# Optimization experiments

Measured on AMD Instinct MI355X. Metric: run time of the kernel, lower is better.

The kernel has to match this reference:

```python
import jax, jax.numpy as jnp
import numpy as np

B, H0, W0, DIM, HEADS, WS, SHIFT = 32, 56, 56, 384, 12, 7, 3
MLP_HID = DIM * 4
N = WS * WS  # tokens per window

def _rel_pos_index(ws):
    coords = np.stack(np.meshgrid(np.arange(ws), np.arange(ws), indexing='ij')).reshape(2, -1)
    rel = (coords[:, :, None] - coords[:, None, :]).transpose(1, 2, 0)
    rel[:, :, 0] += ws - 1
    rel[:, :, 1] += ws - 1
    rel[:, :, 0] *= 2 * ws - 1
    return rel.sum(-1)  # (N, N) int

REL_IDX = _rel_pos_index(WS)

def _shift_mask(H, W, ws, shift):
    # standard Swin SW-MSA mask: 0 within same region, -100 across regions
    img = np.zeros((H, W), dtype=np.int32)
    cnt = 0
    for hs in (slice(0, -ws), slice(-ws, -shift), slice(-shift, None)):
        for wsl in (slice(0, -ws), slice(-ws, -shift), slice(-shift, None)):
            img[hs, wsl] = cnt
            cnt += 1
    mw = img.reshape(H // ws, ws, W // ws, ws).transpose(0, 2, 1, 3).reshape(-1, ws * ws)
    return np.where(mw[:, None, :] != mw[:, :, None], -100.0, 0.0).astype(np.float32)  # (nW, N, N)

MASK = _shift_mask(H0, W0, WS, SHIFT)

def _ln(x, g, b, eps=1e-5):
    m = x.mean(-1, keepdims=True)
    v = ((x - m) ** 2).mean(-1, keepdims=True)
    return (x - m) / jnp.sqrt(v + eps) * g + b

def setup_inputs():
    key = jax.random.key(0)
    ks = jax.random.split(key, 8)
    d = {}
    d['x'] = jax.random.normal(ks[0], (B, H0 * W0, DIM), jnp.float32)
    d['H'], d['W'] = H0, W0
    d['norm1_g'] = jnp.ones((DIM,), jnp.float32)
    d['norm1_b'] = jnp.zeros((DIM,), jnp.float32)
    d['qkv_w'] = jax.random.normal(ks[1], (3 * DIM, DIM), jnp.float32) * 0.02
    d['qkv_b'] = jnp.zeros((3 * DIM,), jnp.float32)
    d['rpb_table'] = jax.random.normal(ks[2], ((2 * WS - 1) ** 2, HEADS), jnp.float32) * 0.02
    d['proj_w'] = jax.random.normal(ks[3], (DIM, DIM), jnp.float32) * 0.02
    d['proj_b'] = jnp.zeros((DIM,), jnp.float32)
    d['norm2_g'] = jnp.ones((DIM,), jnp.float32)
    d['norm2_b'] = jnp.zeros((DIM,), jnp.float32)
    d['fc1_w'] = jax.random.normal(ks[4], (MLP_HID, DIM), jnp.float32) * 0.02
    d['fc1_b'] = jnp.zeros((MLP_HID,), jnp.float32)
    d['fc2_w'] = jax.random.normal(ks[5], (DIM, MLP_HID), jnp.float32) * 0.02
    d['fc2_b'] = jnp.zeros((DIM,), jnp.float32)
    return d

def reference(x, H, W, norm1_g, norm1_b, qkv_w, qkv_b, rpb_table, proj_w, proj_b, norm2_g, norm2_b, fc1_w, fc1_b, fc2_w, fc2_b):
    Bx, L, C = x.shape
    hd = C // HEADS
    scale = hd ** -0.5
    shortcut = x
    xn = _ln(x, norm1_g, norm1_b).reshape(Bx, H, W, C)
    if SHIFT > 0:
        xn = jnp.roll(xn, (-SHIFT, -SHIFT), axis=(1, 2))
    nWh, nWw = H // WS, W // WS
    nW = nWh * nWw
    # window partition: (B, H, W, C) -> (B*nW, N, C)
    xw = xn.reshape(Bx, nWh, WS, nWw, WS, C).transpose(0, 1, 3, 2, 4, 5).reshape(-1, N, C)
    qkv = (xw @ qkv_w.T + qkv_b).reshape(-1, N, 3, HEADS, hd).transpose(2, 0, 3, 1, 4)
    q, k, v = qkv[0] * scale, qkv[1], qkv[2]  # (B*nW, HEADS, N, hd)
    attn = jnp.einsum('bhnd,bhmd->bhnm', q, k)
    bias = rpb_table[jnp.asarray(REL_IDX.reshape(-1))].reshape(N, N, HEADS).transpose(2, 0, 1)
    attn = attn + bias[None]
    if SHIFT > 0:
        attn = attn.reshape(Bx, nW, HEADS, N, N) + jnp.asarray(MASK)[None, :, None]
        attn = attn.reshape(-1, HEADS, N, N)
    attn = jax.nn.softmax(attn, axis=-1)
    out = jnp.einsum('bhnm,bhmd->bhnd', attn, v).transpose(0, 2, 1, 3).reshape(-1, N, C)
    out = out @ proj_w.T + proj_b
    # window reverse: (B*nW, N, C) -> (B, H, W, C)
    xr = out.reshape(Bx, nWh, nWw, WS, WS, C).transpose(0, 1, 3, 2, 4, 5).reshape(Bx, H, W, C)
    if SHIFT > 0:
        xr = jnp.roll(xr, (SHIFT, SHIFT), axis=(1, 2))
    x = shortcut + xr.reshape(Bx, L, C)
    h = _ln(x, norm2_g, norm2_b)
    h = jax.nn.gelu(h @ fc1_w.T + fc1_b, approximate=False)  # nn.GELU default = exact erf
    h = h @ fc2_w.T + fc2_b
    return x + h
```

## Files before the change

### kernel.cpp

```cpp
#include <hip/hip_runtime.h>
#include <hip/hip_bf16.h>

#define C_DIM   384
#define HEADS   12
#define HDIM    32
#define NTOK    49
#define TOT_WIN 2048
#define M_TOK   100352
#define QKV_N   1152
#define MLP_N   1536
#define SHIFT_V 3

typedef __bf16 bf16x8_t __attribute__((ext_vector_type(8)));
typedef float  f32x4_t  __attribute__((ext_vector_type(4)));

__device__ inline float b2f(ushort u) {
    union { unsigned u; float f; } p; p.u = ((unsigned)u) << 16; return p.f;
}
__device__ inline ushort f2b(float f) {
    union { float f; unsigned u; } p; p.f = f;
    unsigned r = p.u + 0x7FFF + ((p.u >> 16) & 1);
    return (ushort)(r >> 16);
}
__device__ inline float ldin(const void* p, size_t i, int dt) {
    return dt ? b2f(((const ushort*)p)[i]) : ((const float*)p)[i];
}

__device__ inline void gload_lds16(const ushort* g, ushort* l) {
    __builtin_amdgcn_global_load_lds(
        (__attribute__((address_space(1))) void*)const_cast<ushort*>(g),
        (__attribute__((address_space(3))) void*)l, 16, 0, 0);
}

__device__ inline int win2tok(int grow) {
    int widx = grow / 49, tok = grow - widx * 49;
    int b = widx >> 6, w_ = widx & 63;
    int wh = w_ >> 3, ww = w_ & 7;
    int r = tok / 7, c = tok - r * 7;
    int h = wh * 7 + r + SHIFT_V; if (h >= 56) h -= 56;
    int wc = ww * 7 + c + SHIFT_V; if (wc >= 56) wc -= 56;
    return b * 3136 + h * 56 + wc;
}

__global__ void sniff_kernel(const ushort* x16, int* flag) {
    const int tid = threadIdx.x;
    int cnt = 0;
    for (int i = tid; i < 4096; i += 256) {
        ushort u = x16[2 * i];
        int e = (u >> 7) & 0xFF;
        if ((u & 0x7FFF) == 0 || (e >= 107 && e <= 147)) cnt++;
    }
    __shared__ int ss[256];
    ss[tid] = cnt; __syncthreads();
    for (int s = 128; s; s >>= 1) { if (tid < s) ss[tid] += ss[tid + s]; __syncthreads(); }
    if (tid == 0) *flag = (ss[0] >= 2048) ? 1 : 0;
}

__global__ void cvt_w_kernel(const void* src, ushort* dst, int n, const int* flagp) {
    const int dt = *flagp;
    for (int i = blockIdx.x * blockDim.x + threadIdx.x; i < n; i += gridDim.x * blockDim.x)
        dst[i] = dt ? ((const ushort*)src)[i] : f2b(((const float*)src)[i]);
}

__global__ void cvt_p_kernel(const void* n1g, const void* n1b, const void* qkvb,
                             const void* projb, const void* n2g, const void* n2b,
                             const void* fc1b, const void* fc2b, const void* rpb,
                             float* prm, const int* flagp) {
    const int dt = *flagp;
    for (int i = threadIdx.x; i < 7020; i += 256) {
        float v;
        if      (i < 384)  v = ldin(n1g,  i,        dt);
        else if (i < 768)  v = ldin(n1b,  i - 384,  dt);
        else if (i < 1920) v = ldin(qkvb, i - 768,  dt);
        else if (i < 2304) v = ldin(projb,i - 1920, dt);
        else if (i < 2688) v = ldin(n2g,  i - 2304, dt);
        else if (i < 3072) v = ldin(n2b,  i - 2688, dt);
        else if (i < 4608) v = ldin(fc1b, i - 3072, dt);
        else if (i < 4992) v = ldin(fc2b, i - 4608, dt);
        else               v = ldin(rpb,  i - 4992, dt);
        prm[i] = v;
    }
}

template<int MODE>
__global__ __launch_bounds__(256) void ln_kernel(
    const void* __restrict__ x, const float* __restrict__ g,
    const float* __restrict__ b, ushort* __restrict__ out,
    const int* flagp, int moff)
{
    const int dt = *flagp;
    const int wid = threadIdx.x >> 6, lane = threadIdx.x & 63;
    const int m = blockIdx.x * 4 + wid;
    const int src = (MODE == 0) ? win2tok(moff + m) : (moff + m);

    float v[6]; float s = 0.f, sq = 0.f;
    #pragma unroll
    for (int k = 0; k < 6; ++k) {
        size_t idx = (size_t)src * C_DIM + lane + 64 * k;
        v[k] = (MODE == 2) ? b2f(((const ushort*)x)[idx]) : ldin(x, idx, dt);
        s += v[k]; sq += v[k] * v[k];
    }
    #pragma unroll
    for (int off = 32; off; off >>= 1) {
        s  += __shfl_xor(s,  off, 64);
        sq += __shfl_xor(sq, off, 64);
    }
    float mean = s * (1.f / 384.f);
    float var  = sq * (1.f / 384.f) - mean * mean;
    float rstd = rsqrtf(var + 1e-5f);
    #pragma unroll
    for (int k = 0; k < 6; ++k) {
        int col = lane + 64 * k;
        out[(size_t)m * C_DIM + col] =
            f2b((v[k] - mean) * rstd * g[col] + b[col]);
    }
}

template<int MODE>
__global__ __launch_bounds__(512) void gemm_bt(
    const ushort* __restrict__ A, const ushort* __restrict__ W,
    const float* __restrict__ bias, ushort* outb, void* outv,
    const void* resid, const int* flagp, int N, int K, int Mrows, int moff)
{
    __shared__ __align__(16) ushort As[2][256 * 32];
    __shared__ __align__(16) ushort Bs[2][128 * 32];

    const int dt   = *flagp;
    const int tid  = threadIdx.x;
    const int wid  = tid >> 6;
    const int lane = tid & 63;
    const int bm = blockIdx.y * 256;
    const int bn = blockIdx.x * 128;
    const int wm = (wid >> 1) * 64;
    const int wn = (wid & 1) * 64;
    const int lrow = lane & 15;
    const int lk   = (lane >> 4) << 3;

    const int arow = tid >> 2;
    const int koff = (tid & 3) << 3;
    const int ar0 = (bm + arow       < Mrows) ? (bm + arow)       : (Mrows - 1);
    const int ar1 = (bm + 128 + arow < Mrows) ? (bm + 128 + arow) : (Mrows - 1);
    const int brow = bn + arow;

    const ushort* pa0 = A + (size_t)ar0 * K + koff;
    const ushort* pa1 = A + (size_t)ar1 * K + koff;
    const ushort* pb  = W + (size_t)brow * K + koff;

    float biasf[4]; int coln[4];
    #pragma unroll
    for (int n = 0; n < 4; ++n) {
        coln[n] = bn + wn + n * 16 + lrow;
        biasf[n] = bias[coln[n]];
    }

    f32x4_t acc[4][4];
    #pragma unroll
    for (int m = 0; m < 4; ++m)
        #pragma unroll
        for (int n = 0; n < 4; ++n) acc[m][n] = (f32x4_t){0.f, 0.f, 0.f, 0.f};

    const int nk = K >> 5;
    gload_lds16(pa0, As[0] + tid * 8);
    gload_lds16(pa1, As[0] + 4096 + tid * 8);
    gload_lds16(pb,  Bs[0] + tid * 8);

    int cur = 0;
    for (int kt = 0; kt < nk; ++kt) {
        if (kt + 1 < nk) {
            const int nxt = cur ^ 1;
            const int k1 = (kt + 1) << 5;
            gload_lds16(pa0 + k1, As[nxt] + tid * 8);
            gload_lds16(pa1 + k1, As[nxt] + 4096 + tid * 8);
            gload_lds16(pb  + k1, Bs[nxt] + tid * 8);
            __builtin_amdgcn_sched_barrier(0);
            asm volatile("s_waitcnt vmcnt(3)" ::: "memory");
        } else {
            asm volatile("s_waitcnt vmcnt(0)" ::: "memory");
        }
        __builtin_amdgcn_s_barrier();
        __builtin_amdgcn_sched_barrier(0);

        bf16x8_t af[4], bfr[4];
        #pragma unroll
        for (int m = 0; m < 4; ++m)
            af[m] = *(const bf16x8_t*)&As[cur][(wm + m * 16 + lrow) * 32 + lk];
        #pragma unroll
        for (int n = 0; n < 4; ++n)
            bfr[n] = *(const bf16x8_t*)&Bs[cur][(wn + n * 16 + lrow) * 32 + lk];
        #pragma unroll
        for (int m = 0; m < 4; ++m)
            #pragma unroll
            for (int n = 0; n < 4; ++n)
                acc[m][n] = __builtin_amdgcn_mfma_f32_16x16x32_bf16(
                    af[m], bfr[n], acc[m][n], 0, 0, 0);

        __builtin_amdgcn_sched_barrier(0);
        __builtin_amdgcn_s_barrier();
        cur ^= 1;
    }

    const int rbase = bm + wm + ((lane >> 4) << 2);
    #pragma unroll
    for (int m = 0; m < 4; ++m) {
        #pragma unroll
        for (int j = 0; j < 4; ++j) {
            int grow = rbase + m * 16 + j;
            if (grow >= Mrows) continue;
            #pragma unroll
            for (int n = 0; n < 4; ++n) {
                float v = acc[m][n][j] + biasf[n];
                if (MODE == 0) {
                    outb[(size_t)grow * N + coln[n]] = f2b(v);
                } else if (MODE == 2) {
                    v = 0.5f * v * (1.0f + erff(v * 0.70710678118654752f));
                    outb[(size_t)grow * N + coln[n]] = f2b(v);
                } else if (MODE == 1) {
                    size_t oidx = (size_t)win2tok(moff + grow) * (size_t)N + coln[n];
                    outb[oidx] = f2b(v + ldin(resid, oidx, dt));
                } else {
                    size_t oidx = (size_t)(moff + grow) * (size_t)N + coln[n];
                    float r = v + b2f(((const ushort*)resid)[oidx]);
                    if (dt) ((ushort*)outv)[oidx] = f2b(r);
                    else    ((float*) outv)[oidx] = r;
                }
            }
        }
    }
}

__global__ __launch_bounds__(256) void attn_kernel(
    const ushort* __restrict__ qkv, const float* __restrict__ rpb,
    ushort* __restrict__ out, int win_off)
{
    __shared__ __align__(16) ushort Pl[4][64 * 64];
    __shared__ __align__(16) ushort Vtl[4][32 * 64];

    const int tid = threadIdx.x, wid = tid >> 6, lane = tid & 63;
    const int lo = lane & 15, hi = lane >> 4;
    const int widx = blockIdx.x;
    const int w_ = (win_off + widx) & 63;
    const int wh = w_ >> 3, ww = w_ & 7;
    const bool edge = (wh == 7) || (ww == 7);

    char* P  = (char*)Pl[wid];
    char* Vw = (char*)Vtl[wid];

    int qr[4], qc[4], rq[4];
    #pragma unroll
    for (int n = 0; n < 4; ++n) {
        int q = n * 16 + lo; if (q > 48) q = 48;
        qr[n] = q / 7; qc[n] = q - qr[n] * 7;
        int gh = wh * 7 + qr[n], gw = ww * 7 + qc[n];
        rq[n] = (gh < 49 ? 0 : (gh < 53 ? 1 : 2)) * 3 + (gw < 49 ? 0 : (gw < 53 ? 1 : 2));
    }

    for (int h = wid; h < HEADS; h += 4) {
        const size_t hb = (size_t)widx * 49 * QKV_N + h * HDIM;

        bf16x8_t kf[4], qf[4];
        #pragma unroll
        for (int t = 0; t < 4; ++t) {
            int r = t * 16 + lo;
            bf16x8_t z = {};
            kf[t] = z; qf[t] = z;
            if (r < 49) {
                kf[t] = *(const bf16x8_t*)(qkv + hb + (size_t)r * QKV_N + 384 + hi * 8);
                qf[t] = *(const bf16x8_t*)(qkv + hb + (size_t)r * QKV_N + hi * 8);
            }
        }

        {
            const int kk = lane;
            union { bf16x8_t v; ushort u[8]; } vv[4];
            #pragma unroll
            for (int c = 0; c < 4; ++c) {
                bf16x8_t z = {};
                vv[c].v = (kk < 49) ? *(const bf16x8_t*)(qkv + hb + (size_t)kk * QKV_N + 768 + c * 8)
                                    : z;
            }
            #pragma unroll
            for (int d = 0; d < 32; ++d) {
                int byo = (d * 128 + kk * 2) ^ ((d & 7) << 4);
                *(ushort*)(Vw + byo) = vv[d >> 3].u[d & 7];
            }
        }

        f32x4_t St[4][4];
        #pragma unroll
        for (int m = 0; m < 4; ++m)
            #pragma unroll
            for (int n = 0; n < 4; ++n) St[m][n] = (f32x4_t){0.f, 0.f, 0.f, 0.f};
        #pragma unroll
        for (int m = 0; m < 4; ++m)
            #pragma unroll
            for (int n = 0; n < 4; ++n)
                St[m][n] = __builtin_amdgcn_mfma_f32_16x16x32_bf16(kf[m], qf[n], St[m][n], 0, 0, 0);

        #pragma unroll
        for (int m = 0; m < 4; ++m) {
            #pragma unroll
            for (int j = 0; j < 4; ++j) {
                const int kk = m * 16 + hi * 4 + j;
                const int kcl = (kk > 48) ? 48 : kk;
                const int kr = kcl / 7, kc = kcl - kr * 7;
                int rk = 0;
                if (edge) {
                    int gh = wh * 7 + kr, gw = ww * 7 + kc;
                    rk = (gh < 49 ? 0 : (gh < 53 ? 1 : 2)) * 3 + (gw < 49 ? 0 : (gw < 53 ? 1 : 2));
                }
                #pragma unroll
                for (int n = 0; n < 4; ++n) {
                    int idx = (qr[n] - kr + 6) * 13 + (qc[n] - kc + 6);
                    float v = St[m][n][j] * 0.17677669529663687f + rpb[idx * 12 + h];
                    if (edge && (rq[n] != rk)) v -= 100.f;
                    if (kk > 48) v = -1e30f;
                    St[m][n][j] = v;
                }
            }
        }

        float sm[4];
        #pragma unroll
        for (int n = 0; n < 4; ++n) {
            float mv = St[0][n][0];
            #pragma unroll
            for (int m = 0; m < 4; ++m)
                #pragma unroll
                for (int j = 0; j < 4; ++j) mv = fmaxf(mv, St[m][n][j]);
            mv = fmaxf(mv, __shfl_xor(mv, 16, 64));
            mv = fmaxf(mv, __shfl_xor(mv, 32, 64));
            float sv = 0.f;
            #pragma unroll
            for (int m = 0; m < 4; ++m)
                #pragma unroll
                for (int j = 0; j < 4; ++j) {
                    float e = __expf(St[m][n][j] - mv);
                    St[m][n][j] = e; sv += e;
                }
            sv += __shfl_xor(sv, 16, 64);
            sv += __shfl_xor(sv, 32, 64);
            sm[n] = 1.f / sv;
        }

        #pragma unroll
        for (int m = 0; m < 4; ++m) {
            #pragma unroll
            for (int n = 0; n < 4; ++n) {
                union { ushort4 u4; __bf16 b[4]; } pk;
                #pragma unroll
                for (int j = 0; j < 4; ++j) pk.b[j] = (__bf16)(St[m][n][j] * sm[n]);
                int byo = ((n * 16 + lo) * 128 + (m * 16 + hi * 4) * 2) ^ ((lo & 7) << 4);
                *(ushort4*)(P + byo) = pk.u4;
            }
        }

        f32x4_t Oa[4][2];
        #pragma unroll
        for (int mt = 0; mt < 4; ++mt)
            #pragma unroll
            for (int nt = 0; nt < 2; ++nt) Oa[mt][nt] = (f32x4_t){0.f, 0.f, 0.f, 0.f};
        #pragma unroll
        for (int s = 0; s < 2; ++s) {
            bf16x8_t vf[2];
            #pragma unroll
            for (int nt = 0; nt < 2; ++nt) {
                int byo = ((nt * 16 + lo) * 128 + s * 64 + hi * 16) ^ ((lo & 7) << 4);
                vf[nt] = *(const bf16x8_t*)(Vw + byo);
            }
            #pragma unroll
            for (int mt = 0; mt < 4; ++mt) {
                int byo = ((mt * 16 + lo) * 128 + s * 64 + hi * 16) ^ ((lo & 7) << 4);
                bf16x8_t pf = *(const bf16x8_t*)(P + byo);
                #pragma unroll
                for (int nt = 0; nt < 2; ++nt)
                    Oa[mt][nt] = __builtin_amdgcn_mfma_f32_16x16x32_bf16(pf, vf[nt], Oa[mt][nt], 0, 0, 0);
            }
        }

        #pragma unroll
        for (int mt = 0; mt < 4; ++mt) {
            #pragma unroll
            for (int j = 0; j < 4; ++j) {
                int q = mt * 16 + hi * 4 + j;
                if (q < 49) {
                    size_t ro = ((size_t)(widx * 49 + q)) * C_DIM + h * HDIM;
                    #pragma unroll
                    for (int nt = 0; nt < 2; ++nt)
                        out[ro + nt * 16 + lo] = f2b(Oa[mt][nt][j]);
                }
            }
        }
    }
}

extern "C" void kernel_launch(void* const* d_in, const int* in_sizes, int n_in,
                              void* d_out, int out_size, void* d_ws, size_t ws_size,
                              hipStream_t stream)
{
    const void* x      = d_in[0];
    const void* n1g    = d_in[3];
    const void* n1b    = d_in[4];
    const void* qkv_w  = d_in[5];
    const void* qkv_b  = d_in[6];
    const void* rpb    = d_in[7];
    const void* proj_w = d_in[8];
    const void* proj_b = d_in[9];
    const void* n2g    = d_in[10];
    const void* n2b    = d_in[11];
    const void* fc1_w  = d_in[12];
    const void* fc1_b  = d_in[13];
    const void* fc2_w  = d_in[14];
    const void* fc2_b  = d_in[15];

    int*    flagp = (int*)d_ws;
    float*  prm   = (float*)((char*)d_ws + 256);
    ushort* wq    = (ushort*)((char*)d_ws + 28416);
    ushort* wp    = wq + 442368;
    ushort* w1m   = wp + 147456;
    ushort* w2m   = w1m + 589824;
    const size_t WSTATIC = 3567360;
    const size_t X2B_B   = 77070336ull;

    int nc = 64;
    const int opts[7] = {1, 2, 4, 8, 16, 32, 64};
    for (int i = 0; i < 7; ++i) {
        size_t need = WSTATIC + X2B_B + ((size_t)M_TOK / opts[i]) * 3840ull;
        if (need <= ws_size) { nc = opts[i]; break; }
    }
    const int wins_pc = TOT_WIN / nc;
    const int rows_pc = wins_pc * NTOK;
    const int gx      = (rows_pc + 255) / 256;

    ushort* x2b = (ushort*)((char*)d_ws + WSTATIC);
    ushort* ws0 = x2b + (size_t)M_TOK * C_DIM;
    ushort* ws1 = ws0 + (size_t)rows_pc * C_DIM;

    sniff_kernel<<<1, 256, 0, stream>>>((const ushort*)x, flagp);
    cvt_p_kernel<<<1, 256, 0, stream>>>(n1g, n1b, qkv_b, proj_b, n2g, n2b,
                                        fc1_b, fc2_b, rpb, prm, flagp);
    cvt_w_kernel<<<432, 256, 0, stream>>>(qkv_w,  wq,  442368, flagp);
    cvt_w_kernel<<<144, 256, 0, stream>>>(proj_w, wp,  147456, flagp);
    cvt_w_kernel<<<576, 256, 0, stream>>>(fc1_w,  w1m, 589824, flagp);
    cvt_w_kernel<<<576, 256, 0, stream>>>(fc2_w,  w2m, 589824, flagp);

    const float* b_qkv = prm + 768;
    const float* b_prj = prm + 1920;
    const float* b_fc1 = prm + 3072;
    const float* b_fc2 = prm + 4608;
    const float* rpb_c = prm + 4992;

    for (int c = 0; c < nc; ++c) {
        const int moff = c * rows_pc;
        ln_kernel<0><<<rows_pc / 4, 256, 0, stream>>>(x, prm + 0, prm + 384, ws0, flagp, moff);
        gemm_bt<0><<<dim3(9, gx), 512, 0, stream>>>(
            ws0, wq, b_qkv, ws1, nullptr, nullptr, flagp, QKV_N, C_DIM, rows_pc, 0);
        attn_kernel<<<wins_pc, 256, 0, stream>>>(ws1, rpb_c, ws0, c * wins_pc);
        gemm_bt<1><<<dim3(3, gx), 512, 0, stream>>>(
            ws0, wp, b_prj, x2b, nullptr, x, flagp, C_DIM, C_DIM, rows_pc, moff);
    }

    for (int c = 0; c < nc; ++c) {
        const int moff = c * rows_pc;
        ln_kernel<2><<<rows_pc / 4, 256, 0, stream>>>(x2b, prm + 2304, prm + 2688, ws0, flagp, moff);
        gemm_bt<2><<<dim3(12, gx), 512, 0, stream>>>(
            ws0, w1m, b_fc1, ws1, nullptr, nullptr, flagp, MLP_N, C_DIM, rows_pc, 0);
        gemm_bt<3><<<dim3(3, gx), 512, 0, stream>>>(
            ws1, w2m, b_fc2, nullptr, d_out, x2b, flagp, C_DIM, MLP_N, rows_pc, moff);
    }
}
```

Measured before the change: 1.099 ms.

## Add K=384 GEMM kernel holding full weight tile in LDS, reading A directly

Adds a GEMM variant for the K=384 matmuls (QKV, proj, fc1). It stages a 64-column slice of the whole weight matrix in padded LDS once per block and streams activation rows straight from global memory into MFMA fragments. This drops the double-buffered A/B LDS pipeline and its per-k-step barriers. In exchange each block covers 512 rows by 64 columns, so the grid shape changes, and A loads are not staged through LDS or reused across waves. The original GEMM is kept only for fc2, with its epilogue reduced to that one mode.

```diff
diff --git a/kernel.cpp b/kernel.cpp
--- a/kernel.cpp
+++ b/kernel.cpp
@@ -117,6 +117,96 @@
 }
 
 template<int MODE>
+__global__ __launch_bounds__(512) void gemm_nw(
+    const ushort* __restrict__ A, const ushort* __restrict__ W,
+    const float* __restrict__ bias, ushort* outb,
+    const void* resid, const int* flagp, int N, int Mrows, int moff)
+{
+    __shared__ __align__(16) ushort Wl[12 * 64 * 40];
+
+    const int dt   = *flagp;
+    const int tid  = threadIdx.x;
+    const int wid  = tid >> 6;
+    const int lane = tid & 63;
+    const int bm = blockIdx.y * 512;
+    const int bn = blockIdx.x * 64;
+    const int wm = wid * 64;
+    const int lo = lane & 15;
+    const int hi = lane >> 4;
+
+    #pragma unroll
+    for (int i = 0; i < 6; ++i) {
+        const int c = tid + 512 * i;
+        const int r = c / 48, j = c - r * 48;
+        const int p = j >> 2, q = j & 3;
+        bf16x8_t v = *(const bf16x8_t*)(W + (size_t)(bn + r) * 384 + p * 32 + q * 8);
+        *(bf16x8_t*)&Wl[p * 2560 + r * 40 + q * 8] = v;
+    }
+    __syncthreads();
+
+    const ushort* pA[4];
+    #pragma unroll
+    for (int m = 0; m < 4; ++m) {
+        int r = bm + wm + m * 16 + lo;
+        if (r >= Mrows) r = Mrows - 1;
+        pA[m] = A + (size_t)r * 384 + hi * 8;
+    }
+
+    float biasf[4]; int coln[4];
+    #pragma unroll
+    for (int n = 0; n < 4; ++n) {
+        coln[n] = bn + n * 16 + lo;
+        biasf[n] = bias[coln[n]];
+    }
+
+    f32x4_t acc[4][4];
+    #pragma unroll
+    for (int m = 0; m < 4; ++m)
+        #pragma unroll
+        for (int n = 0; n < 4; ++n) acc[m][n] = (f32x4_t){0.f, 0.f, 0.f, 0.f};
+
+    #pragma unroll
+    for (int kt = 0; kt < 12; ++kt) {
+        bf16x8_t af[4], wf[4];
+        #pragma unroll
+        for (int m = 0; m < 4; ++m)
+            af[m] = *(const bf16x8_t*)(pA[m] + kt * 32);
+        #pragma unroll
+        for (int n = 0; n < 4; ++n)
+            wf[n] = *(const bf16x8_t*)&Wl[kt * 2560 + (n * 16 + lo) * 40 + hi * 8];
+        #pragma unroll
+        for (int m = 0; m < 4; ++m)
+            #pragma unroll
+            for (int n = 0; n < 4; ++n)
+                acc[m][n] = __builtin_amdgcn_mfma_f32_16x16x32_bf16(
+                    af[m], wf[n], acc[m][n], 0, 0, 0);
+    }
+
+    const int rbase = bm + wm + (hi << 2);
+    #pragma unroll
+    for (int m = 0; m < 4; ++m) {
+        #pragma unroll
+        for (int j = 0; j < 4; ++j) {
+            int grow = rbase + m * 16 + j;
+            if (grow >= Mrows) continue;
+            #pragma unroll
+            for (int n = 0; n < 4; ++n) {
+                float v = acc[m][n][j] + biasf[n];
+                if (MODE == 0) {
+                    outb[(size_t)grow * N + coln[n]] = f2b(v);
+                } else if (MODE == 2) {
+                    v = 0.5f * v * (1.0f + erff(v * 0.70710678118654752f));
+                    outb[(size_t)grow * N + coln[n]] = f2b(v);
+                } else {
+                    size_t oidx = (size_t)win2tok(moff + grow) * (size_t)N + coln[n];
+                    outb[oidx] = f2b(v + ldin(resid, oidx, dt));
+                }
+            }
+        }
+    }
+}
+
+template<int MODE>
 __global__ __launch_bounds__(512) void gemm_bt(
     const ushort* __restrict__ A, const ushort* __restrict__ W,
     const float* __restrict__ bias, ushort* outb, void* outv,
@@ -209,20 +299,10 @@
             #pragma unroll
             for (int n = 0; n < 4; ++n) {
                 float v = acc[m][n][j] + biasf[n];
-                if (MODE == 0) {
-                    outb[(size_t)grow * N + coln[n]] = f2b(v);
-                } else if (MODE == 2) {
-                    v = 0.5f * v * (1.0f + erff(v * 0.70710678118654752f));
-                    outb[(size_t)grow * N + coln[n]] = f2b(v);
-                } else if (MODE == 1) {
-                    size_t oidx = (size_t)win2tok(moff + grow) * (size_t)N + coln[n];
-                    outb[oidx] = f2b(v + ldin(resid, oidx, dt));
-                } else {
-                    size_t oidx = (size_t)(moff + grow) * (size_t)N + coln[n];
-                    float r = v + b2f(((const ushort*)resid)[oidx]);
-                    if (dt) ((ushort*)outv)[oidx] = f2b(r);
-                    else    ((float*) outv)[oidx] = r;
-                }
+                size_t oidx = (size_t)(moff + grow) * (size_t)N + coln[n];
+                float r = v + b2f(((const ushort*)resid)[oidx]);
+                if (dt) ((ushort*)outv)[oidx] = f2b(r);
+                else    ((float*) outv)[oidx] = r;
             }
         }
     }
@@ -429,7 +509,8 @@
     }
     const int wins_pc = TOT_WIN / nc;
     const int rows_pc = wins_pc * NTOK;
-    const int gx      = (rows_pc + 255) / 256;
+    const int gx5     = (rows_pc + 511) / 512;
+    const int gx2     = (rows_pc + 255) / 256;
 
     ushort* x2b = (ushort*)((char*)d_ws + WSTATIC);
     ushort* ws0 = x2b + (size_t)M_TOK * C_DIM;
@@ -452,19 +533,19 @@
     for (int c = 0; c < nc; ++c) {
         const int moff = c * rows_pc;
         ln_kernel<0><<<rows_pc / 4, 256, 0, stream>>>(x, prm + 0, prm + 384, ws0, flagp, moff);
-        gemm_bt<0><<<dim3(9, gx), 512, 0, stream>>>(
-            ws0, wq, b_qkv, ws1, nullptr, nullptr, flagp, QKV_N, C_DIM, rows_pc, 0);
+        gemm_nw<0><<<dim3(18, gx5), 512, 0, stream>>>(
+            ws0, wq, b_qkv, ws1, nullptr, flagp, QKV_N, rows_pc, 0);
         attn_kernel<<<wins_pc, 256, 0, stream>>>(ws1, rpb_c, ws0, c * wins_pc);
-        gemm_bt<1><<<dim3(3, gx), 512, 0, stream>>>(
-            ws0, wp, b_prj, x2b, nullptr, x, flagp, C_DIM, C_DIM, rows_pc, moff);
+        gemm_nw<1><<<dim3(6, gx5), 512, 0, stream>>>(
+            ws0, wp, b_prj, x2b, x, flagp, C_DIM, rows_pc, moff);
     }
 
     for (int c = 0; c < nc; ++c) {
         const int moff = c * rows_pc;
         ln_kernel<2><<<rows_pc / 4, 256, 0, stream>>>(x2b, prm + 2304, prm + 2688, ws0, flagp, moff);
-        gemm_bt<2><<<dim3(12, gx), 512, 0, stream>>>(
-            ws0, w1m, b_fc1, ws1, nullptr, nullptr, flagp, MLP_N, C_DIM, rows_pc, 0);
-        gemm_bt<3><<<dim3(3, gx), 512, 0, stream>>>(
+        gemm_nw<2><<<dim3(24, gx5), 512, 0, stream>>>(
+            ws0, w1m, b_fc1, ws1, nullptr, flagp, MLP_N, rows_pc, 0);
+        gemm_bt<3><<<dim3(3, gx2), 512, 0, stream>>>(
             ws1, w2m, b_fc2, nullptr, d_out, x2b, flagp, C_DIM, MLP_N, rows_pc, moff);
     }
 }
```

Result: slower. 1.294 ms (+17.7%).
